# Kernel optimization log

Hardware: AMD Instinct MI355X
Metric: run time of the kernel (lower is better)

Reference implementation:

```python
import jax, jax.numpy as jnp
import numpy as np

N, E, C, H, IN = 100000, 800000, 47, 128, 128
ALPHA, THETA, RSL = 0.1, 0.5, 0.5
L = 4


def setup_inputs() -> dict:
    key = jax.random.key(0)
    ks = jax.random.split(key, 11)
    x = jax.random.normal(ks[0], (N, IN), jnp.float32)
    edge_index = jax.random.randint(ks[1], (2, E), 0, N, dtype=jnp.int32)
    edge_weight = jax.random.uniform(ks[2], (E,), jnp.float32)
    label = jax.random.randint(ks[3], (N,), 0, C, dtype=jnp.int32)
    p = jax.random.uniform(ks[4], (N, C), jnp.float32)
    cm = jax.random.normal(ks[5], (C, 1, C), jnp.float32)
    lin0_w = jax.random.normal(ks[6], (IN, H), jnp.float32) * 0.05
    lin0_b = jnp.zeros((H,), jnp.float32)
    lin1_w = jax.random.normal(ks[7], (H, C), jnp.float32) * 0.05
    lin1_b = jnp.zeros((C,), jnp.float32)
    conv_w = jax.random.normal(ks[8], (L, H, H), jnp.float32) * 0.05  # glorot-ish scale
    return {"x": x, "edge_index": edge_index, "edge_weight": edge_weight,
            "label": label, "p": p, "cm": cm,
            "lin0_w": lin0_w, "lin0_b": lin0_b,
            "lin1_w": lin1_w, "lin1_b": lin1_b, "conv_w": conv_w}


def _gcn2_forward(x, edge_index, edge_weight, label, p, cm,
                  lin0_w, lin0_b, lin1_w, lin1_b, conv_w):
    src, dst = edge_index[0], edge_index[1]
    # input linear + relu (dropout p=0 -> identity)
    x = jax.nn.relu(x @ lin0_w + lin0_b)
    x0 = x
    ones_n = jnp.ones((N,), x.dtype)
    for i in range(L):
        beta = float(np.log(THETA / (i + 1) + 1.0))
        # sparse propagate: sum_j edge_weight_ij * x_j  (aggr='add')
        msgs = x[src] * edge_weight[:, None]          # [E, H]
        out = jax.ops.segment_sum(msgs, dst, num_segments=N)  # [N, H]
        # --- RSL branch (rsl > 0) ---
        s = x + 0.1 * x0
        sums = jax.ops.segment_sum(s, label, num_segments=C)       # [C, H]
        cnt = jax.ops.segment_sum(ones_n, label, num_segments=C)   # [C]
        centers = jax.lax.stop_gradient(sums / jnp.maximum(cnt, 1.0)[:, None])
        r = centers[:, None, :] - centers[None, :, :]  # [C, C, H], r[i,j]=c_i-c_j
        rn = jnp.linalg.norm(r, axis=-1, keepdims=True)
        rn = jnp.where(rn == 0, jnp.ones_like(rn), rn)
        r = r / rn
        r = jnp.matmul(cm, r).squeeze(1)  # [C,1,C] @ [C,C,H] -> [C,1,H] -> [C,H]
        r = p @ r                         # [N, H]
        a = out - x
        out = x + RSL * r + (1.0 - RSL) * a
        # identity mapping + initial residual (shared_weights=True)
        out = out * (1.0 - ALPHA) + ALPHA * x0
        out = (1.0 - beta) * out + beta * (out @ conv_w[i])
        x = jax.nn.relu(out)
    return x @ lin1_w + lin1_b  # [N, C]


def reference(x, edge_index, edge_weight, label, p, cm,
              lin0_w, lin0_b, lin1_w, lin1_b, conv_w):
    return _gcn2_forward(x, edge_index, edge_weight, label, p, cm,
                         lin0_w, lin0_b, lin1_w, lin1_b, conv_w)
```

## Files before the change

### kernel.cpp

```cpp
#include <hip/hip_runtime.h>
#include <math.h>

#define NN 100000
#define EE 800000
#define CC 47
#define HH 128
#define NB 391
#define CHUNK 2000

typedef __attribute__((ext_vector_type(8))) short short8v;
typedef __attribute__((ext_vector_type(4))) float float4v;

__device__ inline ushort f2bf(float f) {
    unsigned u = __float_as_uint(f);
    unsigned r = (u + 0x7fffu + ((u >> 16) & 1u)) >> 16;
    return (ushort)r;
}
__device__ inline float b2f(ushort u) { return __uint_as_float(((unsigned)u) << 16); }

__global__ __launch_bounds__(256) void hist_kernel(const int* __restrict__ dst,
                                                   int* __restrict__ deg, int e) {
    int i = blockIdx.x * 256 + threadIdx.x;
    if (i < e) atomicAdd(&deg[dst[i]], 1);
}

__global__ __launch_bounds__(256) void scan_block_kernel(const int* __restrict__ deg,
                                                         int* __restrict__ rowptr,
                                                         int* __restrict__ bsum, int n) {
    __shared__ int ls[256];
    int b = blockIdx.x, t = threadIdx.x;
    int i0 = b * 512 + 2 * t;
    int a0 = (i0 < n) ? deg[i0] : 0;
    int a1 = (i0 + 1 < n) ? deg[i0 + 1] : 0;
    int val = a0 + a1;
    ls[t] = val;
    __syncthreads();
    for (int off = 1; off < 256; off <<= 1) {
        int add = (t >= off) ? ls[t - off] : 0;
        __syncthreads();
        val += add;
        ls[t] = val;
        __syncthreads();
    }
    int incl1 = val;
    int incl0 = val - a1;
    if (i0 < n) rowptr[i0 + 1] = incl0;
    if (i0 + 1 < n) rowptr[i0 + 2] = incl1;
    if (t == 255) bsum[b] = val;
}

__global__ __launch_bounds__(256) void scan_bsum_kernel(int* __restrict__ bsum, int nb) {
    __shared__ int ls[256];
    int t = threadIdx.x;
    int v = (t < nb) ? bsum[t] : 0;
    int orig = v;
    ls[t] = v;
    __syncthreads();
    for (int off = 1; off < 256; off <<= 1) {
        int add = (t >= off) ? ls[t - off] : 0;
        __syncthreads();
        v += add;
        ls[t] = v;
        __syncthreads();
    }
    if (t < nb) bsum[t] = v - orig;
}

__global__ __launch_bounds__(256) void add_off_kernel(int* __restrict__ rowptr,
                                                      const int* __restrict__ bsum, int n) {
    int i = blockIdx.x * 256 + threadIdx.x;
    if (i < n) rowptr[i + 1] += bsum[i >> 9];
    if (i == 0) rowptr[0] = 0;
}

__global__ __launch_bounds__(256) void init_bcur_kernel(const int* __restrict__ rowptr,
                                                        int* __restrict__ bcur) {
    int b = blockIdx.x * 256 + threadIdx.x;
    if (b < 512) bcur[b] = rowptr[min(b * 256, NN)];
}

__global__ __launch_bounds__(256) void coarse_fill_kernel(const int* __restrict__ src,
                                                          const int* __restrict__ dst,
                                                          const float* __restrict__ ew,
                                                          int* __restrict__ bcur,
                                                          int2* __restrict__ stage, int e) {
    __shared__ int hist[512];
    __shared__ int base_local[512];
    __shared__ int gbase[512];
    __shared__ int lc[512];
    __shared__ int ls[256];
    __shared__ int2 le[CHUNK];
    __shared__ ushort lb[CHUNK];
    int t = threadIdx.x;
    int beg = blockIdx.x * CHUNK, end = min(e, beg + CHUNK);
    int cnt = end - beg;
    for (int i = t; i < 512; i += 256) { hist[i] = 0; lc[i] = 0; }
    __syncthreads();
    for (int i = beg + t; i < end; i += 256) atomicAdd(&hist[((unsigned)dst[i]) >> 8], 1);
    __syncthreads();
    int a0 = hist[2 * t], a1 = hist[2 * t + 1];
    int val = a0 + a1;
    ls[t] = val;
    __syncthreads();
    for (int off = 1; off < 256; off <<= 1) {
        int add = (t >= off) ? ls[t - off] : 0;
        __syncthreads();
        val += add;
        ls[t] = val;
        __syncthreads();
    }
    base_local[2 * t] = val - a0 - a1;
    base_local[2 * t + 1] = val - a1;
    __syncthreads();
    for (int b = t; b < 512; b += 256)
        if (hist[b] > 0) gbase[b] = atomicAdd(&bcur[b], hist[b]);
    __syncthreads();
    for (int i = beg + t; i < end; i += 256) {
        int d = dst[i];
        int bk = ((unsigned)d) >> 8;
        int slot = base_local[bk] + atomicAdd(&lc[bk], 1);
        le[slot] = make_int2(((d & 255) << 24) | src[i], __float_as_int(ew[i]));
        lb[slot] = (ushort)bk;
    }
    __syncthreads();
    for (int s = t; s < cnt; s += 256) {
        int bk = lb[s];
        stage[gbase[bk] + (s - base_local[bk])] = le[s];
    }
}

__global__ __launch_bounds__(256) void fine_fill_kernel(const int2* __restrict__ stage,
                                                        const int* __restrict__ rowptr,
                                                        int2* __restrict__ csr, int n) {
    __shared__ int cur[256];
    __shared__ int rp[257];
    int b = blockIdx.x, t = threadIdx.x;
    int node0 = b * 256;
    int nodes = min(256, n - node0);
    cur[t] = 0;
    rp[t] = rowptr[min(node0 + t, n)];
    if (t == 0) rp[256] = rowptr[min(node0 + 256, n)];
    __syncthreads();
    int S = rp[0], E = rp[nodes];
    for (int i = S + t; i < E; i += 256) {
        int2 en = stage[i];
        int dl = ((unsigned)en.x) >> 24;
        int pos = rp[dl] + atomicAdd(&cur[dl], 1);
        csr[pos] = make_int2(en.x & 0xFFFFFF, en.y);
    }
}

__global__ __launch_bounds__(256) void lhist_kernel(const int* __restrict__ label,
                                                    int* __restrict__ lcnt, int n) {
    __shared__ int lh[CC];
    if (threadIdx.x < CC) lh[threadIdx.x] = 0;
    __syncthreads();
    for (int i = blockIdx.x * 256 + threadIdx.x; i < n; i += gridDim.x * 256)
        atomicAdd(&lh[label[i]], 1);
    __syncthreads();
    if (threadIdx.x < CC) atomicAdd(&lcnt[threadIdx.x], lh[threadIdx.x]);
}

__global__ __launch_bounds__(64) void lscan_kernel(const int* __restrict__ lcnt,
                                                   int* __restrict__ lbase,
                                                   int* __restrict__ gcur,
                                                   float* __restrict__ cntf) {
    __shared__ int ls[CC];
    int t = threadIdx.x;
    if (t < CC) {
        int v = lcnt[t];
        cntf[t] = (float)v;
        gcur[t] = 0;
        ls[t] = v;
    }
    __syncthreads();
    if (t == 0) {
        int run = 0;
        for (int c = 0; c < CC; c++) { int x = ls[c]; ls[c] = run; run += x; }
    }
    __syncthreads();
    if (t < CC) lbase[t] = ls[t];
}

__global__ __launch_bounds__(256) void lfill_kernel(const int* __restrict__ label,
                                                    const int* __restrict__ lbase,
                                                    int* __restrict__ gcur,
                                                    int* __restrict__ perm, int n) {
    __shared__ int lh[CC], lbs[CC], lc[CC];
    int t = threadIdx.x;
    if (t < CC) lh[t] = 0;
    __syncthreads();
    int chunk = (n + gridDim.x - 1) / gridDim.x;
    int beg = blockIdx.x * chunk, end = min(n, beg + chunk);
    for (int i = beg + t; i < end; i += 256) atomicAdd(&lh[label[i]], 1);
    __syncthreads();
    if (t < CC) {
        lbs[t] = (lh[t] > 0) ? atomicAdd(&gcur[t], lh[t]) : 0;
        lc[t] = 0;
    }
    __syncthreads();
    for (int i = beg + t; i < end; i += 256) {
        int c = label[i];
        int pos = atomicAdd(&lc[c], 1);
        perm[lbase[c] + lbs[c] + pos] = (c << 24) | i;
    }
}

__global__ __launch_bounds__(256) void psum_kernel(const ushort* __restrict__ xb,
                                                   const int* __restrict__ perm,
                                                   float* __restrict__ sums, int n) {
    const int lane = threadIdx.x & 63;
    const int wid = threadIdx.x >> 6;
    int gw = blockIdx.x * 4 + wid;
    int nw = gridDim.x * 4;
    int per = (n + nw - 1) / nw;
    int beg = gw * per, end = min(n, beg + per);
    if (beg >= end) return;
    float ax = 0.0f, ay = 0.0f;
    int ccur = __builtin_amdgcn_readfirstlane(perm[beg]) >> 24;
    int i = beg;
    while (i < end) {
        if (i + 4 <= end) {
            int p0 = __builtin_amdgcn_readfirstlane(perm[i]);
            int p1 = __builtin_amdgcn_readfirstlane(perm[i + 1]);
            int p2 = __builtin_amdgcn_readfirstlane(perm[i + 2]);
            int p3 = __builtin_amdgcn_readfirstlane(perm[i + 3]);
            if ((p0 >> 24) == (p3 >> 24)) {
                int c = p0 >> 24;
                if (c != ccur) {
                    atomicAdd(&sums[ccur * HH + 2 * lane], ax);
                    atomicAdd(&sums[ccur * HH + 2 * lane + 1], ay);
                    ax = ay = 0.0f;
                    ccur = c;
                }
                ushort2 v0 = *(const ushort2*)(xb + (size_t)(p0 & 0xFFFFFF) * HH + 2 * lane);
                ushort2 v1 = *(const ushort2*)(xb + (size_t)(p1 & 0xFFFFFF) * HH + 2 * lane);
                ushort2 v2 = *(const ushort2*)(xb + (size_t)(p2 & 0xFFFFFF) * HH + 2 * lane);
                ushort2 v3 = *(const ushort2*)(xb + (size_t)(p3 & 0xFFFFFF) * HH + 2 * lane);
                ax += b2f(v0.x) + b2f(v1.x) + b2f(v2.x) + b2f(v3.x);
                ay += b2f(v0.y) + b2f(v1.y) + b2f(v2.y) + b2f(v3.y);
                i += 4;
                continue;
            }
        }
        int pe = __builtin_amdgcn_readfirstlane(perm[i]);
        int c = pe >> 24;
        if (c != ccur) {
            atomicAdd(&sums[ccur * HH + 2 * lane], ax);
            atomicAdd(&sums[ccur * HH + 2 * lane + 1], ay);
            ax = ay = 0.0f;
            ccur = c;
        }
        ushort2 v = *(const ushort2*)(xb + (size_t)(pe & 0xFFFFFF) * HH + 2 * lane);
        ax += b2f(v.x);
        ay += b2f(v.y);
        i += 1;
    }
    atomicAdd(&sums[ccur * HH + 2 * lane], ax);
    atomicAdd(&sums[ccur * HH + 2 * lane + 1], ay);
}

__global__ __launch_bounds__(256) void pack_w_kernel(const float* __restrict__ W,
                                                     ushort* __restrict__ Wp) {
    int idx = blockIdx.x * 256 + threadIdx.x;
    int k = idx >> 7, c = idx & 127;
    Wp[(k >> 3) * 1024 + c * 8 + (k & 7)] = f2bf(W[idx]);
}

__global__ __launch_bounds__(256) void pack_w1_kernel(const float* __restrict__ W1,
                                                      ushort* __restrict__ Wp1) {
    int idx = blockIdx.x * 256 + threadIdx.x;
    if (idx >= 6144) return;
    int ksub = idx / 384, rem = idx - ksub * 384;
    int c = rem >> 3, kk = ksub * 8 + (rem & 7);
    Wp1[idx] = (c < CC) ? f2bf(W1[kk * CC + c]) : (ushort)0;
}

__global__ __launch_bounds__(256) void lin0_mfma_kernel(const float* __restrict__ xin,
                                                        const ushort* __restrict__ Wp,
                                                        const float* __restrict__ bias,
                                                        ushort* __restrict__ x0b,
                                                        ushort* __restrict__ xb) {
    __shared__ ushort ts[32 * 128];
    __shared__ ushort wl[128 * 128];
    {
        const uint4* g4 = (const uint4*)Wp;
        uint4* l4 = (uint4*)wl;
        for (int j = threadIdx.x; j < 2048; j += 256) l4[j] = g4[j];
    }
    const int lane = threadIdx.x & 63, wv = threadIdx.x >> 6;
    const int sub = lane >> 4, r16 = lane & 15;
    const int wbase = wv * 32;
    const int rowbase = blockIdx.x * 32;
    const float* tp = xin + (size_t)rowbase * HH;
    #pragma unroll
    for (int j = 0; j < 4; j++) {
        int e = 4 * threadIdx.x + j * 1024;
        float4 f = *(const float4*)(tp + e);
        int r = e >> 7, c = e & 127;
        ushort4 b4 = make_ushort4(f2bf(f.x), f2bf(f.y), f2bf(f.z), f2bf(f.w));
        int off = (r * 256 + c * 2) ^ ((r & 7) << 4);
        *(ushort4*)((char*)ts + off) = b4;
    }
    __syncthreads();
    float4v acc[2][2] = {};
    {
        const char* tsc = (const char*)ts;
        const int sw = (r16 & 7) << 4;
        #pragma unroll
        for (int ks = 0; ks < 4; ks++) {
            short8v a0 = *(const short8v*)(tsc + ((r16 * 256 + ks * 64 + sub * 16) ^ sw));
            short8v a1 = *(const short8v*)(tsc + (((16 + r16) * 256 + ks * 64 + sub * 16) ^ sw));
            int kb = (ks * 4 + sub) * 1024;
            short8v b0 = *(const short8v*)(wl + kb + (wbase + r16) * 8);
            short8v b1 = *(const short8v*)(wl + kb + (wbase + 16 + r16) * 8);
            acc[0][0] = __builtin_amdgcn_mfma_f32_16x16x32_bf16(a0, b0, acc[0][0], 0, 0, 0);
            acc[0][1] = __builtin_amdgcn_mfma_f32_16x16x32_bf16(a0, b1, acc[0][1], 0, 0, 0);
            acc[1][0] = __builtin_amdgcn_mfma_f32_16x16x32_bf16(a1, b0, acc[1][0], 0, 0, 0);
            acc[1][1] = __builtin_amdgcn_mfma_f32_16x16x32_bf16(a1, b1, acc[1][1], 0, 0, 0);
        }
    }
    float bv[2] = {bias[wbase + r16], bias[wbase + 16 + r16]};
    #pragma unroll
    for (int mi = 0; mi < 2; mi++)
        #pragma unroll
        for (int ni = 0; ni < 2; ni++) {
            int col = wbase + ni * 16 + r16;
            #pragma unroll
            for (int r = 0; r < 4; r++) {
                int row = rowbase + mi * 16 + sub * 4 + r;
                float v = fmaxf(acc[mi][ni][r] + bv[ni], 0.0f);
                ushort bv16 = f2bf(v);
                x0b[(size_t)row * HH + col] = bv16;
                xb[(size_t)row * HH + col] = bv16;
            }
        }
}

__global__ __launch_bounds__(64) void cr_kernel(const float* __restrict__ sumsx,
                                                const float* __restrict__ sums0,
                                                const float* __restrict__ cnt,
                                                const float* __restrict__ cm,
                                                ushort* __restrict__ rlp) {
    __shared__ float cs[CC * HH];
    int i = blockIdx.x, lane = threadIdx.x;
    for (int idx = lane; idx < CC * HH; idx += 64) {
        int c = idx >> 7;
        cs[idx] = (sumsx[idx] + 0.1f * sums0[idx]) / fmaxf(cnt[c], 1.0f);
    }
    __syncthreads();
    float ci0 = cs[i * HH + lane];
    float ci1 = cs[i * HH + 64 + lane];
    float acc0 = 0.0f, acc1 = 0.0f;
    for (int j = 0; j < CC; j++) {
        float d0 = ci0 - cs[j * HH + lane];
        float d1 = ci1 - cs[j * HH + 64 + lane];
        float s = d0 * d0 + d1 * d1;
        #pragma unroll
        for (int off = 32; off >= 1; off >>= 1) s += __shfl_xor(s, off);
        float nrm = sqrtf(s);
        if (nrm == 0.0f) nrm = 1.0f;
        float w = cm[i * CC + j] / nrm;
        acc0 = fmaf(w, d0, acc0);
        acc1 = fmaf(w, d1, acc1);
    }
    rlp[(i >> 3) * 1024 + lane * 8 + (i & 7)] = f2bf(acc0);
    rlp[(i >> 3) * 1024 + (lane + 64) * 8 + (i & 7)] = f2bf(acc1);
}

template <int FINAL>
__global__ __launch_bounds__(512, 8) void layer_kernel(
    const ushort* __restrict__ xin, const ushort* __restrict__ x0b,
    const float* __restrict__ p, const ushort* __restrict__ rlp,
    const int* __restrict__ rowptr, const int2* __restrict__ csr,
    const ushort* __restrict__ Wp,
    const ushort* __restrict__ Wp1, const float* __restrict__ b1,
    ushort* __restrict__ xout, float* __restrict__ out, float beta) {
    __shared__ ushort ts[32 * 128];
    __shared__ ushort ps[32 * 64];
    __shared__ ushort prs[32 * 128];
    const int lane = threadIdx.x & 63;
    const int wv = __builtin_amdgcn_readfirstlane(threadIdx.x >> 6);
    const int rowbase = blockIdx.x * 32;
    const int sub = lane >> 4, r16 = lane & 15;
    const int sw = (r16 & 7) << 4;
    if (threadIdx.x < 256) {
        int t = threadIdx.x;
        int r = t >> 3, kc = (t & 7) * 8;
        const float* prow = p + (size_t)(rowbase + r) * CC;
        short8v v;
        #pragma unroll
        for (int j = 0; j < 8; j++) {
            int k = kc + j;
            v[j] = (short)((k < CC) ? f2bf(prow[k]) : (ushort)0);
        }
        int off = (r * 128 + kc * 2) ^ ((r & 7) << 4);
        *(short8v*)((char*)ps + off) = v;
    }
    __syncthreads();
    {
        const char* psc = (const char*)ps;
        float4v pacc[2] = {};
        #pragma unroll
        for (int ks = 0; ks < 2; ks++) {
            short8v a0 = *(const short8v*)(psc + ((r16 * 128 + ks * 64 + sub * 16) ^ sw));
            short8v a1 = *(const short8v*)(psc + (((16 + r16) * 128 + ks * 64 + sub * 16) ^ sw));
            short8v bb = *(const short8v*)(rlp + (ks * 4 + sub) * 1024 + (16 * wv + r16) * 8);
            pacc[0] = __builtin_amdgcn_mfma_f32_16x16x32_bf16(a0, bb, pacc[0], 0, 0, 0);
            pacc[1] = __builtin_amdgcn_mfma_f32_16x16x32_bf16(a1, bb, pacc[1], 0, 0, 0);
        }
        int col = 16 * wv + r16;
        #pragma unroll
        for (int mi = 0; mi < 2; mi++)
            #pragma unroll
            for (int r = 0; r < 4; r++) {
                int rl_ = mi * 16 + sub * 4 + r;
                *(ushort*)((char*)prs + ((rl_ * 256 + col * 2) ^ ((rl_ & 7) << 4))) =
                    f2bf(pacc[mi][r]);
            }
    }
    __syncthreads();
    const int nn0 = rowbase + 4 * wv;
    int rp0 = __builtin_amdgcn_readfirstlane(rowptr[nn0]);
    int rp1 = __builtin_amdgcn_readfirstlane(rowptr[nn0 + 1]);
    int rp2 = __builtin_amdgcn_readfirstlane(rowptr[nn0 + 2]);
    int rp3 = __builtin_amdgcn_readfirstlane(rowptr[nn0 + 3]);
    int rp4 = __builtin_amdgcn_readfirstlane(rowptr[nn0 + 4]);
    int rps[5] = {rp0, rp1, rp2, rp3, rp4};
    #pragma unroll 1
    for (int k = 0; k < 4; k++) {
        int rloc = 4 * wv + k;
        int nn = nn0 + k;
        int beg = rps[k], end = rps[k + 1];
        float accx = 0.0f, accy = 0.0f;
        int e2 = beg;
        for (; e2 + 8 <= end; e2 += 8) {
            int2 ed[8];
            #pragma unroll
            for (int u = 0; u < 8; u++) ed[u] = csr[e2 + u];
            ushort2 vv[8];
            #pragma unroll
            for (int u = 0; u < 8; u++)
                vv[u] = *(const ushort2*)(xin + (size_t)ed[u].x * HH + 2 * lane);
            #pragma unroll
            for (int u = 0; u < 8; u++) {
                float w = __int_as_float(ed[u].y);
                accx = fmaf(w, b2f(vv[u].x), accx);
                accy = fmaf(w, b2f(vv[u].y), accy);
            }
        }
        for (; e2 + 4 <= end; e2 += 4) {
            int2 ed[4];
            #pragma unroll
            for (int u = 0; u < 4; u++) ed[u] = csr[e2 + u];
            ushort2 vv[4];
            #pragma unroll
            for (int u = 0; u < 4; u++)
                vv[u] = *(const ushort2*)(xin + (size_t)ed[u].x * HH + 2 * lane);
            #pragma unroll
            for (int u = 0; u < 4; u++) {
                float w = __int_as_float(ed[u].y);
                accx = fmaf(w, b2f(vv[u].x), accx);
                accy = fmaf(w, b2f(vv[u].y), accy);
            }
        }
        for (; e2 < end; e2++) {
            int2 ed = csr[e2];
            ushort2 v = *(const ushort2*)(xin + (size_t)ed.x * HH + 2 * lane);
            float w = __int_as_float(ed.y);
            accx = fmaf(w, b2f(v.x), accx);
            accy = fmaf(w, b2f(v.y), accy);
        }
        int poff = (rloc * 256 + lane * 4) ^ ((rloc & 7) << 4);
        ushort2 pv = *(const ushort2*)((const char*)prs + poff);
        ushort2 xc = *(const ushort2*)(xin + (size_t)nn * HH + 2 * lane);
        ushort2 xo = *(const ushort2*)(x0b + (size_t)nn * HH + 2 * lane);
        ushort2 o;
        o.x = f2bf(0.45f * b2f(xc.x) + 0.45f * b2f(pv.x) + 0.45f * accx + 0.1f * b2f(xo.x));
        o.y = f2bf(0.45f * b2f(xc.y) + 0.45f * b2f(pv.y) + 0.45f * accy + 0.1f * b2f(xo.y));
        *(ushort2*)((char*)ts + poff) = o;
    }
    __syncthreads();
    const char* tsc = (const char*)ts;
    float4v acc[2] = {};
    #pragma unroll
    for (int ks = 0; ks < 4; ks++) {
        short8v a0 = *(const short8v*)(tsc + ((r16 * 256 + ks * 64 + sub * 16) ^ sw));
        short8v a1 = *(const short8v*)(tsc + (((16 + r16) * 256 + ks * 64 + sub * 16) ^ sw));
        short8v bb = *(const short8v*)(Wp + (ks * 4 + sub) * 1024 + (16 * wv + r16) * 8);
        acc[0] = __builtin_amdgcn_mfma_f32_16x16x32_bf16(a0, bb, acc[0], 0, 0, 0);
        acc[1] = __builtin_amdgcn_mfma_f32_16x16x32_bf16(a1, bb, acc[1], 0, 0, 0);
    }
    const float omb = 1.0f - beta;
    const int col = 16 * wv + r16;
    if constexpr (!FINAL) {
        #pragma unroll
        for (int mi = 0; mi < 2; mi++)
            #pragma unroll
            for (int r = 0; r < 4; r++) {
                int rl_ = mi * 16 + sub * 4 + r;
                int toff = (rl_ * 256 + col * 2) ^ ((rl_ & 7) << 4);
                float tv = b2f(*(const ushort*)(tsc + toff));
                float v = fmaxf(omb * tv + beta * acc[mi][r], 0.0f);
                xout[(size_t)(rowbase + rl_) * HH + col] = f2bf(v);
            }
    } else {
        __syncthreads();
        #pragma unroll
        for (int mi = 0; mi < 2; mi++)
            #pragma unroll
            for (int r = 0; r < 4; r++) {
                int rl_ = mi * 16 + sub * 4 + r;
                int toff = (rl_ * 256 + col * 2) ^ ((rl_ & 7) << 4);
                ushort* slot = (ushort*)((char*)ts + toff);
                float tv = b2f(*slot);
                float v = fmaxf(omb * tv + beta * acc[mi][r], 0.0f);
                *slot = f2bf(v);
            }
        __syncthreads();
        if (wv < 3) {
            float4v a2[2] = {};
            #pragma unroll
            for (int ks = 0; ks < 4; ks++) {
                short8v a0 = *(const short8v*)(tsc + ((r16 * 256 + ks * 64 + sub * 16) ^ sw));
                short8v a1 = *(const short8v*)(tsc + (((16 + r16) * 256 + ks * 64 + sub * 16) ^ sw));
                short8v bb = *(const short8v*)(Wp1 + (ks * 4 + sub) * 384 + (wv * 16 + r16) * 8);
                a2[0] = __builtin_amdgcn_mfma_f32_16x16x32_bf16(a0, bb, a2[0], 0, 0, 0);
                a2[1] = __builtin_amdgcn_mfma_f32_16x16x32_bf16(a1, bb, a2[1], 0, 0, 0);
            }
            int col2 = wv * 16 + r16;
            if (col2 < CC) {
                float bias = b1[col2];
                #pragma unroll
                for (int mi = 0; mi < 2; mi++)
                    #pragma unroll
                    for (int r = 0; r < 4; r++) {
                        int row = rowbase + mi * 16 + sub * 4 + r;
                        out[(size_t)row * CC + col2] = a2[mi][r] + bias;
                    }
            }
        }
    }
}

extern "C" void kernel_launch(void* const* d_in, const int* in_sizes, int n_in,
                              void* d_out, int out_size, void* d_ws, size_t ws_size,
                              hipStream_t stream) {
    const float* x_in   = (const float*)d_in[0];
    const int*   ei     = (const int*)d_in[1];
    const float* ew     = (const float*)d_in[2];
    const int*   label  = (const int*)d_in[3];
    const float* p      = (const float*)d_in[4];
    const float* cm     = (const float*)d_in[5];
    const float* lin0_w = (const float*)d_in[6];
    const float* lin0_b = (const float*)d_in[7];
    const float* lin1_w = (const float*)d_in[8];
    const float* lin1_b = (const float*)d_in[9];
    const float* conv_w = (const float*)d_in[10];
    float* out = (float*)d_out;

    const int* src = ei;
    const int* dst = ei + EE;

    const size_t NH = (size_t)NN * HH;
    float* ws = (float*)d_ws;
    float* cnt   = ws;
    float* sums0 = cnt + 64;
    float* sumsx = sums0 + CC * HH;
    int*   deg    = (int*)(sumsx + CC * HH);
    int*   rowptr = deg + NN;
    int*   bsum   = rowptr + NN + 64;
    int*   bcur   = bsum + 256;
    int*   lcnt   = bcur + 512;
    int*   lbase  = lcnt + 64;
    int*   gcur   = lbase + 64;
    int*   perm   = gcur + 64;
    int2*  csr    = (int2*)(perm + NN);
    int2*  stage  = csr + EE;
    ushort* x0b   = (ushort*)(stage + EE);
    ushort* xbA   = x0b + NH;
    ushort* xbB   = xbA + NH;
    ushort* wp0   = xbB + NH;
    ushort* wpc   = wp0 + 16384;
    ushort* wp1   = wpc + 4 * 16384;
    ushort* rlp   = wp1 + 8192;

    hipMemsetAsync(deg, 0, NN * sizeof(int), stream);
    hist_kernel<<<(EE + 255) / 256, 256, 0, stream>>>(dst, deg, EE);
    const int NBLK = (NN + 511) / 512;
    scan_block_kernel<<<NBLK, 256, 0, stream>>>(deg, rowptr, bsum, NN);
    scan_bsum_kernel<<<1, 256, 0, stream>>>(bsum, NBLK);
    add_off_kernel<<<(NN + 255) / 256, 256, 0, stream>>>(rowptr, bsum, NN);
    init_bcur_kernel<<<2, 256, 0, stream>>>(rowptr, bcur);
    coarse_fill_kernel<<<(EE + CHUNK - 1) / CHUNK, 256, 0, stream>>>(src, dst, ew, bcur, stage, EE);
    fine_fill_kernel<<<NB, 256, 0, stream>>>(stage, rowptr, csr, NN);

    hipMemsetAsync(lcnt, 0, CC * sizeof(int), stream);
    lhist_kernel<<<256, 256, 0, stream>>>(label, lcnt, NN);
    lscan_kernel<<<1, 64, 0, stream>>>(lcnt, lbase, gcur, cnt);
    lfill_kernel<<<256, 256, 0, stream>>>(label, lbase, gcur, perm, NN);

    pack_w_kernel<<<64, 256, 0, stream>>>(lin0_w, wp0);
    for (int i = 0; i < 4; i++)
        pack_w_kernel<<<64, 256, 0, stream>>>(conv_w + (size_t)i * HH * HH, wpc + (size_t)i * 16384);
    pack_w1_kernel<<<24, 256, 0, stream>>>(lin1_w, wp1);
    hipMemsetAsync(rlp, 0, 8192 * sizeof(ushort), stream);

    lin0_mfma_kernel<<<NN / 32, 256, 0, stream>>>(x_in, wp0, lin0_b, x0b, xbA);

    hipMemsetAsync(sums0, 0, CC * HH * sizeof(float), stream);
    psum_kernel<<<2048, 256, 0, stream>>>(x0b, perm, sums0, NN);

    const float betas[4] = {logf(0.5f / 1.0f + 1.0f), logf(0.5f / 2.0f + 1.0f),
                            logf(0.5f / 3.0f + 1.0f), logf(0.5f / 4.0f + 1.0f)};

    ushort* xin_b = xbA;
    ushort* xout_b = xbB;
    for (int i = 0; i < 4; i++) {
        if (i == 0) {
            cr_kernel<<<CC, 64, 0, stream>>>(sums0, sums0, cnt, cm, rlp);
        } else {
            hipMemsetAsync(sumsx, 0, CC * HH * sizeof(float), stream);
            psum_kernel<<<2048, 256, 0, stream>>>(xin_b, perm, sumsx, NN);
            cr_kernel<<<CC, 64, 0, stream>>>(sumsx, sums0, cnt, cm, rlp);
        }
        if (i < 3) {
            layer_kernel<0><<<NN / 32, 512, 0, stream>>>(xin_b, x0b, p, rlp, rowptr, csr,
                                                         wpc + (size_t)i * 16384, wp1, lin1_b,
                                                         xout_b, out, betas[i]);
            ushort* tmp = xin_b; xin_b = xout_b; xout_b = tmp;
        } else {
            layer_kernel<1><<<NN / 32, 512, 0, stream>>>(xin_b, x0b, p, rlp, rowptr, csr,
                                                         wpc + 3 * 16384, wp1, lin1_b,
                                                         xout_b, out, betas[3]);
        }
    }
}
```

Measured before the change: 558.0 us.

## Merge memsets and weight packing, flatten per-wave SpMM gather, drop LDS weight copy

Replaces the separate memsets with a single zero kernel over a reorganised workspace and gives each layer its own center-sum buffer, so per-layer memsets are no longer needed. The six weight-packing launches become one kernel. lin0 now reads packed weights straight from global memory instead of staging 32KB into LDS, which lowers LDS use and may raise occupancy. The layer kernel's gather loop now walks a wave's four rows as one contiguous edge range with branchy per-row accumulators, improving unrolling over short rows at the cost of extra compare and branch work per edge.

```diff
diff --git a/kernel.cpp b/kernel.cpp
--- a/kernel.cpp
+++ b/kernel.cpp
@@ -7,6 +7,7 @@
 #define HH 128
 #define NB 391
 #define CHUNK 2000
+#define CH (CC * HH)
 
 typedef __attribute__((ext_vector_type(8))) short short8v;
 typedef __attribute__((ext_vector_type(4))) float float4v;
@@ -17,6 +18,10 @@
     return (ushort)r;
 }
 __device__ inline float b2f(ushort u) { return __uint_as_float(((unsigned)u) << 16); }
+
+__global__ __launch_bounds__(256) void zero_kernel(int* __restrict__ z, int n) {
+    for (int i = blockIdx.x * 256 + threadIdx.x; i < n; i += gridDim.x * 256) z[i] = 0;
+}
 
 __global__ __launch_bounds__(256) void hist_kernel(const int* __restrict__ dst,
                                                    int* __restrict__ deg, int e) {
@@ -260,20 +265,28 @@
     atomicAdd(&sums[ccur * HH + 2 * lane + 1], ay);
 }
 
-__global__ __launch_bounds__(256) void pack_w_kernel(const float* __restrict__ W,
-                                                     ushort* __restrict__ Wp) {
+__global__ __launch_bounds__(256) void pack_all_kernel(const float* __restrict__ lin0_w,
+                                                       const float* __restrict__ conv_w,
+                                                       const float* __restrict__ W1,
+                                                       ushort* __restrict__ wp0,
+                                                       ushort* __restrict__ wpc,
+                                                       ushort* __restrict__ wp1) {
     int idx = blockIdx.x * 256 + threadIdx.x;
-    int k = idx >> 7, c = idx & 127;
-    Wp[(k >> 3) * 1024 + c * 8 + (k & 7)] = f2bf(W[idx]);
-}
-
-__global__ __launch_bounds__(256) void pack_w1_kernel(const float* __restrict__ W1,
-                                                      ushort* __restrict__ Wp1) {
-    int idx = blockIdx.x * 256 + threadIdx.x;
-    if (idx >= 6144) return;
-    int ksub = idx / 384, rem = idx - ksub * 384;
-    int c = rem >> 3, kk = ksub * 8 + (rem & 7);
-    Wp1[idx] = (c < CC) ? f2bf(W1[kk * CC + c]) : (ushort)0;
+    if (idx < 5 * 16384) {
+        int m = idx >> 14;
+        int r = idx & 16383;
+        int k = r >> 7, c = r & 127;
+        const float* W = (m == 0) ? lin0_w : conv_w + (size_t)(m - 1) * 16384;
+        ushort* Wp = (m == 0) ? wp0 : wpc + (size_t)(m - 1) * 16384;
+        Wp[(k >> 3) * 1024 + c * 8 + (k & 7)] = f2bf(W[r]);
+    } else {
+        int j = idx - 5 * 16384;
+        if (j < 6144) {
+            int ksub = j / 384, rem = j - ksub * 384;
+            int c = rem >> 3, kk = ksub * 8 + (rem & 7);
+            wp1[j] = (c < CC) ? f2bf(W1[kk * CC + c]) : (ushort)0;
+        }
+    }
 }
 
 __global__ __launch_bounds__(256) void lin0_mfma_kernel(const float* __restrict__ xin,
@@ -282,12 +295,6 @@
                                                         ushort* __restrict__ x0b,
                                                         ushort* __restrict__ xb) {
     __shared__ ushort ts[32 * 128];
-    __shared__ ushort wl[128 * 128];
-    {
-        const uint4* g4 = (const uint4*)Wp;
-        uint4* l4 = (uint4*)wl;
-        for (int j = threadIdx.x; j < 2048; j += 256) l4[j] = g4[j];
-    }
     const int lane = threadIdx.x & 63, wv = threadIdx.x >> 6;
     const int sub = lane >> 4, r16 = lane & 15;
     const int wbase = wv * 32;
@@ -312,8 +319,8 @@
             short8v a0 = *(const short8v*)(tsc + ((r16 * 256 + ks * 64 + sub * 16) ^ sw));
             short8v a1 = *(const short8v*)(tsc + (((16 + r16) * 256 + ks * 64 + sub * 16) ^ sw));
             int kb = (ks * 4 + sub) * 1024;
-            short8v b0 = *(const short8v*)(wl + kb + (wbase + r16) * 8);
-            short8v b1 = *(const short8v*)(wl + kb + (wbase + 16 + r16) * 8);
+            short8v b0 = *(const short8v*)(Wp + kb + (wbase + r16) * 8);
+            short8v b1 = *(const short8v*)(Wp + kb + (wbase + 16 + r16) * 8);
             acc[0][0] = __builtin_amdgcn_mfma_f32_16x16x32_bf16(a0, b0, acc[0][0], 0, 0, 0);
             acc[0][1] = __builtin_amdgcn_mfma_f32_16x16x32_bf16(a0, b1, acc[0][1], 0, 0, 0);
             acc[1][0] = __builtin_amdgcn_mfma_f32_16x16x32_bf16(a1, b0, acc[1][0], 0, 0, 0);
@@ -426,59 +433,52 @@
     int rp2 = __builtin_amdgcn_readfirstlane(rowptr[nn0 + 2]);
     int rp3 = __builtin_amdgcn_readfirstlane(rowptr[nn0 + 3]);
     int rp4 = __builtin_amdgcn_readfirstlane(rowptr[nn0 + 4]);
-    int rps[5] = {rp0, rp1, rp2, rp3, rp4};
-    #pragma unroll 1
-    for (int k = 0; k < 4; k++) {
-        int rloc = 4 * wv + k;
-        int nn = nn0 + k;
-        int beg = rps[k], end = rps[k + 1];
-        float accx = 0.0f, accy = 0.0f;
-        int e2 = beg;
-        for (; e2 + 8 <= end; e2 += 8) {
-            int2 ed[8];
-            #pragma unroll
-            for (int u = 0; u < 8; u++) ed[u] = csr[e2 + u];
-            ushort2 vv[8];
-            #pragma unroll
-            for (int u = 0; u < 8; u++)
-                vv[u] = *(const ushort2*)(xin + (size_t)ed[u].x * HH + 2 * lane);
-            #pragma unroll
-            for (int u = 0; u < 8; u++) {
-                float w = __int_as_float(ed[u].y);
-                accx = fmaf(w, b2f(vv[u].x), accx);
-                accy = fmaf(w, b2f(vv[u].y), accy);
-            }
-        }
-        for (; e2 + 4 <= end; e2 += 4) {
-            int2 ed[4];
-            #pragma unroll
-            for (int u = 0; u < 4; u++) ed[u] = csr[e2 + u];
-            ushort2 vv[4];
-            #pragma unroll
-            for (int u = 0; u < 4; u++)
-                vv[u] = *(const ushort2*)(xin + (size_t)ed[u].x * HH + 2 * lane);
-            #pragma unroll
-            for (int u = 0; u < 4; u++) {
-                float w = __int_as_float(ed[u].y);
-                accx = fmaf(w, b2f(vv[u].x), accx);
-                accy = fmaf(w, b2f(vv[u].y), accy);
-            }
-        }
-        for (; e2 < end; e2++) {
-            int2 ed = csr[e2];
-            ushort2 v = *(const ushort2*)(xin + (size_t)ed.x * HH + 2 * lane);
-            float w = __int_as_float(ed.y);
-            accx = fmaf(w, b2f(v.x), accx);
-            accy = fmaf(w, b2f(v.y), accy);
-        }
-        int poff = (rloc * 256 + lane * 4) ^ ((rloc & 7) << 4);
-        ushort2 pv = *(const ushort2*)((const char*)prs + poff);
-        ushort2 xc = *(const ushort2*)(xin + (size_t)nn * HH + 2 * lane);
-        ushort2 xo = *(const ushort2*)(x0b + (size_t)nn * HH + 2 * lane);
-        ushort2 o;
-        o.x = f2bf(0.45f * b2f(xc.x) + 0.45f * b2f(pv.x) + 0.45f * accx + 0.1f * b2f(xo.x));
-        o.y = f2bf(0.45f * b2f(xc.y) + 0.45f * b2f(pv.y) + 0.45f * accy + 0.1f * b2f(xo.y));
-        *(ushort2*)((char*)ts + poff) = o;
+    float ax0 = 0, ay0 = 0, ax1 = 0, ay1 = 0, ax2 = 0, ay2 = 0, ax3 = 0, ay3 = 0;
+#define ACC_EDGE(IDX, W, FX, FY)                                          \
+    if ((IDX) < rp1) { ax0 = fmaf(W, FX, ax0); ay0 = fmaf(W, FY, ay0); }  \
+    else if ((IDX) < rp2) { ax1 = fmaf(W, FX, ax1); ay1 = fmaf(W, FY, ay1); } \
+    else if ((IDX) < rp3) { ax2 = fmaf(W, FX, ax2); ay2 = fmaf(W, FY, ay2); } \
+    else { ax3 = fmaf(W, FX, ax3); ay3 = fmaf(W, FY, ay3); }
+    int e2 = rp0;
+    for (; e2 + 8 <= rp4; e2 += 8) {
+        int2 ed[8];
+        #pragma unroll
+        for (int u = 0; u < 8; u++) ed[u] = csr[e2 + u];
+        ushort2 vv[8];
+        #pragma unroll
+        for (int u = 0; u < 8; u++)
+            vv[u] = *(const ushort2*)(xin + (size_t)ed[u].x * HH + 2 * lane);
+        #pragma unroll
+        for (int u = 0; u < 8; u++) {
+            float w = __int_as_float(ed[u].y);
+            float fx = b2f(vv[u].x), fy = b2f(vv[u].y);
+            ACC_EDGE(e2 + u, w, fx, fy)
+        }
+    }
+    for (; e2 < rp4; e2++) {
+        int2 ed = csr[e2];
+        ushort2 v = *(const ushort2*)(xin + (size_t)ed.x * HH + 2 * lane);
+        float w = __int_as_float(ed.y);
+        float fx = b2f(v.x), fy = b2f(v.y);
+        ACC_EDGE(e2, w, fx, fy)
+    }
+#undef ACC_EDGE
+    {
+        float axs[4] = {ax0, ax1, ax2, ax3};
+        float ays[4] = {ay0, ay1, ay2, ay3};
+        #pragma unroll
+        for (int k = 0; k < 4; k++) {
+            int rloc = 4 * wv + k;
+            int nn = nn0 + k;
+            int poff = (rloc * 256 + lane * 4) ^ ((rloc & 7) << 4);
+            ushort2 pv = *(const ushort2*)((const char*)prs + poff);
+            ushort2 xc = *(const ushort2*)(xin + (size_t)nn * HH + 2 * lane);
+            ushort2 xo = *(const ushort2*)(x0b + (size_t)nn * HH + 2 * lane);
+            ushort2 o;
+            o.x = f2bf(0.45f * b2f(xc.x) + 0.45f * b2f(pv.x) + 0.45f * axs[k] + 0.1f * b2f(xo.x));
+            o.y = f2bf(0.45f * b2f(xc.y) + 0.45f * b2f(pv.y) + 0.45f * ays[k] + 0.1f * b2f(xo.y));
+            *(ushort2*)((char*)ts + poff) = o;
+        }
     }
     __syncthreads();
     const char* tsc = (const char*)ts;
@@ -564,15 +564,17 @@
 
     const size_t NH = (size_t)NN * HH;
     float* ws = (float*)d_ws;
-    float* cnt   = ws;
-    float* sums0 = cnt + 64;
-    float* sumsx = sums0 + CC * HH;
-    int*   deg    = (int*)(sumsx + CC * HH);
-    int*   rowptr = deg + NN;
+    float* sums0  = ws;
+    float* sumsxs = sums0 + CH;
+    ushort* rlp   = (ushort*)(sumsxs + 3 * CH);
+    int*   deg    = (int*)(rlp + 8192);
+    int*   lcnt   = deg + NN;
+    const int ZTOT = CH + 3 * CH + 4096 + NN + 64;
+    float* cnt    = (float*)(lcnt + 64);
+    int*   rowptr = (int*)(cnt + 64);
     int*   bsum   = rowptr + NN + 64;
     int*   bcur   = bsum + 256;
-    int*   lcnt   = bcur + 512;
-    int*   lbase  = lcnt + 64;
+    int*   lbase  = bcur + 512;
     int*   gcur   = lbase + 64;
     int*   perm   = gcur + 64;
     int2*  csr    = (int2*)(perm + NN);
@@ -583,9 +585,9 @@
     ushort* wp0   = xbB + NH;
     ushort* wpc   = wp0 + 16384;
     ushort* wp1   = wpc + 4 * 16384;
-    ushort* rlp   = wp1 + 8192;
-
-    hipMemsetAsync(deg, 0, NN * sizeof(int), stream);
+
+    zero_kernel<<<512, 256, 0, stream>>>((int*)ws, ZTOT);
+
     hist_kernel<<<(EE + 255) / 256, 256, 0, stream>>>(dst, deg, EE);
     const int NBLK = (NN + 511) / 512;
     scan_block_kernel<<<NBLK, 256, 0, stream>>>(deg, rowptr, bsum, NN);
@@ -595,20 +597,15 @@
     coarse_fill_kernel<<<(EE + CHUNK - 1) / CHUNK, 256, 0, stream>>>(src, dst, ew, bcur, stage, EE);
     fine_fill_kernel<<<NB, 256, 0, stream>>>(stage, rowptr, csr, NN);
 
-    hipMemsetAsync(lcnt, 0, CC * sizeof(int), stream);
     lhist_kernel<<<256, 256, 0, stream>>>(label, lcnt, NN);
     lscan_kernel<<<1, 64, 0, stream>>>(lcnt, lbase, gcur, cnt);
     lfill_kernel<<<256, 256, 0, stream>>>(label, lbase, gcur, perm, NN);
 
-    pack_w_kernel<<<64, 256, 0, stream>>>(lin0_w, wp0);
-    for (int i = 0; i < 4; i++)
-        pack_w_kernel<<<64, 256, 0, stream>>>(conv_w + (size_t)i * HH * HH, wpc + (size_t)i * 16384);
-    pack_w1_kernel<<<24, 256, 0, stream>>>(lin1_w, wp1);
-    hipMemsetAsync(rlp, 0, 8192 * sizeof(ushort), stream);
+    pack_all_kernel<<<(5 * 16384 + 6144 + 255) / 256, 256, 0, stream>>>(
+        lin0_w, conv_w, lin1_w, wp0, wpc, wp1);
 
     lin0_mfma_kernel<<<NN / 32, 256, 0, stream>>>(x_in, wp0, lin0_b, x0b, xbA);
 
-    hipMemsetAsync(sums0, 0, CC * HH * sizeof(float), stream);
     psum_kernel<<<2048, 256, 0, stream>>>(x0b, perm, sums0, NN);
 
     const float betas[4] = {logf(0.5f / 1.0f + 1.0f), logf(0.5f / 2.0f + 1.0f),
@@ -620,9 +617,9 @@
         if (i == 0) {
             cr_kernel<<<CC, 64, 0, stream>>>(sums0, sums0, cnt, cm, rlp);
         } else {
-            hipMemsetAsync(sumsx, 0, CC * HH * sizeof(float), stream);
-            psum_kernel<<<2048, 256, 0, stream>>>(xin_b, perm, sumsx, NN);
-            cr_kernel<<<CC, 64, 0, stream>>>(sumsx, sums0, cnt, cm, rlp);
+            float* sx = sumsxs + (size_t)(i - 1) * CH;
+            psum_kernel<<<2048, 256, 0, stream>>>(xin_b, perm, sx, NN);
+            cr_kernel<<<CC, 64, 0, stream>>>(sx, sums0, cnt, cm, rlp);
         }
         if (i < 3) {
             layer_kernel<0><<<NN / 32, 512, 0, stream>>>(xin_b, x0b, p, rlp, rowptr, csr,
```

New measurement: 527.2 us. 5.5% less time.
